# Performance work log

Measured on AMD Instinct MI355X. Metric: run time of the kernel, lower is better.

## Reference

```python
import jax, jax.numpy as jnp
import numpy as np
import math

B, S, D_MODEL, D_K = 4, 4096, 1024, 256

def setup_inputs() -> dict:
    key = jax.random.key(0)
    ks = jax.random.split(key, 9)
    def xavier(k, shape):
        fan_out, fan_in = shape
        limit = math.sqrt(6.0 / (fan_in + fan_out))
        return jax.random.uniform(k, shape, jnp.float32, -limit, limit)
    return {
        "_q": jax.random.normal(ks[0], (B, S, D_MODEL), jnp.float32),
        "_k": jax.random.normal(ks[1], (B, S, D_MODEL), jnp.float32),
        "_v": jax.random.normal(ks[2], (B, S, D_MODEL), jnp.float32),
        "mask": jnp.ones((B, 1, S), dtype=bool),  # unused by the original forward
        "Wq": xavier(ks[3], (D_K, D_MODEL)),
        "bq": jnp.zeros((D_K,), jnp.float32),
        "Wk": xavier(ks[4], (D_K, D_MODEL)),
        "bk": jnp.zeros((D_K,), jnp.float32),
        "Wv": xavier(ks[5], (D_K, D_MODEL)),
        "bv": jnp.zeros((D_K,), jnp.float32),
    }

def reference(_q, _k, _v, mask, Wq, bq, Wk, bk, Wv, bv):
    # Linear projections: x @ W.T + b  (torch nn.Linear semantics)
    q = jnp.einsum('bsm,km->bsk', _q, Wq) + bq  # [B,S,d_k]
    k = jnp.einsum('bsm,km->bsk', _k, Wk) + bk
    v = jnp.einsum('bsm,km->bsk', _v, Wv) + bv
    scores = jnp.einsum('bqk,bsk->bqs', q, k) / math.sqrt(D_K)  # [B,S,S]
    atten = jax.nn.softmax(scores, axis=-1)
    out = jnp.einsum('bqs,bsk->bqk', atten, v)  # [B,S,d_k]
    return out
```

## Files before the change

kernel.cpp:

```cpp
#include <hip/hip_runtime.h>
#include <stdint.h>

#define DEV static __device__ __forceinline__

typedef __bf16 bf16x8 __attribute__((ext_vector_type(8)));
typedef float f32x4 __attribute__((ext_vector_type(4)));

typedef const __attribute__((address_space(1))) void* as1cp;
typedef __attribute__((address_space(3))) void* as3p;

DEV uint32_t pk2(float lo, float hi) {
  uint16_t a = __builtin_bit_cast(uint16_t, (__bf16)lo);
  uint16_t b = __builtin_bit_cast(uint16_t, (__bf16)hi);
  return (uint32_t)a | ((uint32_t)b << 16);
}
DEV uint16_t bfc(float f) { return __builtin_bit_cast(uint16_t, (__bf16)f); }
DEV float bf2f(uint32_t h) { return __builtin_bit_cast(float, h << 16); }

DEV void gll16(const void* g, void* l) {
  __builtin_amdgcn_global_load_lds((as1cp)g, (as3p)l, 16, 0, 0);
}

__global__ __launch_bounds__(256, 3) void proj_kernel(
    const float* __restrict__ xq, const float* __restrict__ xk, const float* __restrict__ xv,
    const float* __restrict__ wq, const float* __restrict__ wk, const float* __restrict__ wv,
    const float* __restrict__ bq, const float* __restrict__ bk, const float* __restrict__ bv,
    uint16_t* __restrict__ qo, uint16_t* __restrict__ ko, uint16_t* __restrict__ vo)
{
  const int z = blockIdx.z;
  const float* X  = (z == 0) ? xq : (z == 1) ? xk : xv;
  const float* W  = (z == 0) ? wq : (z == 1) ? wk : wv;
  const float* Bi = (z == 0) ? bq : (z == 1) ? bk : bv;

  const int tid = threadIdx.x;
  const int lane = tid & 63;
  const int w = tid >> 6;
  const int wm = w >> 1, wn = w & 1;
  const int l15 = lane & 15, g = lane >> 4;
  const int m0 = blockIdx.x * 128;
  const int n0 = blockIdx.y * 128;

  __shared__ uint16_t sA[128 * 64];
  __shared__ uint16_t sB[128 * 64];

  const int srow = tid >> 4;
  const int scu  = tid & 15;
  const float* Abase = X + (size_t)(m0 + srow) * 1024 + scu * 4;
  const float* Wbase = W + (size_t)(n0 + srow) * 1024 + scu * 4;
  uint32_t sdst[8];
  #pragma unroll
  for (int r = 0; r < 8; ++r) {
    uint32_t row = (uint32_t)(r * 16 + srow);
    sdst[r] = row * 128 + (((uint32_t)scu * 8) ^ ((row & 7) << 4));
  }

  f32x4 acc[4][4];
  #pragma unroll
  for (int i = 0; i < 4; ++i)
    #pragma unroll
    for (int j = 0; j < 4; ++j) { f32x4 zz = {0.f, 0.f, 0.f, 0.f}; acc[i][j] = zz; }

  float4 a4[8];
  #pragma unroll
  for (int r = 0; r < 8; ++r)
    a4[r] = *(const float4*)(Abase + (size_t)r * 16384);

  for (int kt = 0; kt < 16; ++kt) {
    if (kt) __syncthreads();
    #pragma unroll
    for (int r = 0; r < 8; ++r) {
      uint2 p; p.x = pk2(a4[r].x, a4[r].y); p.y = pk2(a4[r].z, a4[r].w);
      *(uint2*)((char*)sA + sdst[r]) = p;
    }
    {
      float4 w4[8];
      #pragma unroll
      for (int r = 0; r < 8; ++r)
        w4[r] = *(const float4*)(Wbase + (size_t)r * 16384 + kt * 64);
      #pragma unroll
      for (int r = 0; r < 8; ++r) {
        uint2 p; p.x = pk2(w4[r].x, w4[r].y); p.y = pk2(w4[r].z, w4[r].w);
        *(uint2*)((char*)sB + sdst[r]) = p;
      }
    }
    __syncthreads();
    if (kt < 15) {
      #pragma unroll
      for (int r = 0; r < 8; ++r)
        a4[r] = *(const float4*)(Abase + (size_t)r * 16384 + (kt + 1) * 64);
    }
    #pragma unroll
    for (int ks = 0; ks < 2; ++ks) {
      bf16x8 fa[4], fb[4];
      #pragma unroll
      for (int f = 0; f < 4; ++f) {
        uint32_t row = wm * 64 + 16 * f + l15;
        fa[f] = *(const bf16x8*)((char*)sA + row * 128 +
                 (((uint32_t)(ks * 64 + g * 16)) ^ ((row & 7) << 4)));
      }
      #pragma unroll
      for (int f = 0; f < 4; ++f) {
        uint32_t row = wn * 64 + 16 * f + l15;
        fb[f] = *(const bf16x8*)((char*)sB + row * 128 +
                 (((uint32_t)(ks * 64 + g * 16)) ^ ((row & 7) << 4)));
      }
      #pragma unroll
      for (int fm = 0; fm < 4; ++fm)
        #pragma unroll
        for (int fn = 0; fn < 4; ++fn)
          acc[fm][fn] = __builtin_amdgcn_mfma_f32_16x16x32_bf16(fa[fm], fb[fn], acc[fm][fn], 0, 0, 0);
    }
  }

  #pragma unroll
  for (int fn = 0; fn < 4; ++fn) {
    const int n = n0 + wn * 64 + 16 * fn + l15;
    const float bias = Bi[n];
    #pragma unroll
    for (int fm = 0; fm < 4; ++fm) {
      const int mg = m0 + wm * 64 + 16 * fm + 4 * g;
      if (z == 0) {
        #pragma unroll
        for (int r = 0; r < 4; ++r)
          qo[(size_t)(mg + r) * 256 + n] =
              bfc((acc[fm][fn][r] + bias) * 0.09016844f);
      } else if (z == 1) {
        #pragma unroll
        for (int r = 0; r < 4; ++r)
          ko[(size_t)(mg + r) * 256 + n] = bfc(acc[fm][fn][r] + bias);
      } else {
        uint2 pv;
        pv.x = pk2(acc[fm][fn][0] + bias, acc[fm][fn][1] + bias);
        pv.y = pk2(acc[fm][fn][2] + bias, acc[fm][fn][3] + bias);
        *(uint2*)(vo + (((size_t)(mg >> 12)) << 20) + (((size_t)n) << 12) + (mg & 4095)) = pv;
      }
    }
  }
}

__global__ __launch_bounds__(512) void attn_kernel(
    const uint16_t* __restrict__ qg, const uint16_t* __restrict__ kg,
    const uint16_t* __restrict__ vg, float* __restrict__ out)
{
  extern __shared__ char smem[];

  const int bid = blockIdx.x;
  const int xcd = bid & 7, slot = bid >> 3;
  const int batch = xcd >> 1;
  const int q0 = (((xcd & 1) << 5) + slot) * 64;

  const int tid = threadIdx.x;
  const int lane = tid & 63;
  const int w = tid >> 6;
  const int hv = w >> 2;
  const int wq = w & 3;
  const int l15 = lane & 15, g = lane >> 4;
  const size_t rowb = (size_t)batch * 4096;

  bf16x8 qf[8];
  {
    const uint16_t* qp = qg + (rowb + q0 + wq * 16 + l15) * 256;
    #pragma unroll
    for (int ks = 0; ks < 8; ++ks) qf[ks] = *(const bf16x8*)(qp + ks * 32 + g * 8);
  }

  f32x4 o[16];
  #pragma unroll
  for (int i = 0; i < 16; ++i) { f32x4 zz = {0.f, 0.f, 0.f, 0.f}; o[i] = zz; }
  float mrow[4], lrow[4];
  #pragma unroll
  for (int r = 0; r < 4; ++r) { mrow[r] = -1e30f; lrow[r] = 0.f; }

  const char* kgb = (const char*)(kg + rowb * 256);
  const char* vgb = (const char*)(vg + (size_t)batch * 256 * 4096);

  uint32_t kOff[2][2], vOff[2][2], dOff[2];
  #pragma unroll
  for (int i = 0; i < 2; ++i) {
    uint32_t L = (uint32_t)(i * 512 + tid) * 16;
    dOff[i] = L;
    uint32_t row = L >> 9;
    uint32_t colsw = (L & 511) ^ ((row & 7) << 4);
    uint32_t fd = L >> 10, g2 = (L >> 8) & 3, lv = (L >> 4) & 15;
    #pragma unroll
    for (int h = 0; h < 2; ++h) {
      kOff[h][i] = (h * 32 + row) * 512 + colsw;
      vOff[h][i] = (fd * 16 + lv) * 8192 + (h * 32 + g2 * 8) * 2;
    }
  }

  auto STAGE = [&](int buf, int t) {
    const char* kt_ = kgb + (size_t)t * 32768;
    const char* vt_ = vgb + (size_t)t * 128;
    #pragma unroll
    for (int h = 0; h < 2; ++h) {
      char* kd = smem + (size_t)(h * 2 + buf) * 16384;
      char* vd = smem + 65536 + (size_t)(h * 2 + buf) * 16384;
      #pragma unroll
      for (int i = 0; i < 2; ++i) {
        gll16(kt_ + kOff[h][i], kd + dOff[i]);
        gll16(vt_ + vOff[h][i], vd + dOff[i]);
      }
    }
  };

  STAGE(0, 0);
  int buf = 0;
  const int hb = hv * 2;
  char* Pw = smem + 131072 + (size_t)w * 1024;

  for (int t = 0; t < 64; ++t) {
    __syncthreads();
    if (t + 1 < 64) STAGE(buf ^ 1, t + 1);

    const char* Kb = smem + (size_t)(hb + buf) * 16384;
    const char* Vb = smem + 65536 + (size_t)(hb + buf) * 16384;

    f32x4 s4[2];
    #pragma unroll
    for (int f = 0; f < 2; ++f) { f32x4 zz = {0.f, 0.f, 0.f, 0.f}; s4[f] = zz; }
    #pragma unroll
    for (int ks = 0; ks < 8; ++ks) {
      bf16x8 kf[2];
      #pragma unroll
      for (int f = 0; f < 2; ++f) {
        uint32_t row = 16 * f + l15;
        kf[f] = *(const bf16x8*)(Kb + row * 512 +
                 (((uint32_t)(ks * 64 + g * 16)) ^ ((l15 & 7) << 4)));
      }
      #pragma unroll
      for (int f = 0; f < 2; ++f)
        s4[f] = __builtin_amdgcn_mfma_f32_16x16x32_bf16(qf[ks], kf[f], s4[f], 0, 0, 0);
    }

    float mx[4];
    #pragma unroll
    for (int r = 0; r < 4; ++r) {
      float m2 = fmaxf(s4[0][r], s4[1][r]);
      m2 = fmaxf(m2, __shfl_xor(m2, 1, 64));
      m2 = fmaxf(m2, __shfl_xor(m2, 2, 64));
      m2 = fmaxf(m2, __shfl_xor(m2, 4, 64));
      m2 = fmaxf(m2, __shfl_xor(m2, 8, 64));
      mx[r] = m2;
    }
    int stable = (mx[0] <= mrow[0] + 8.f) && (mx[1] <= mrow[1] + 8.f) &&
                 (mx[2] <= mrow[2] + 8.f) && (mx[3] <= mrow[3] + 8.f);
    if (!__all(stable)) {
      float sc[4];
      #pragma unroll
      for (int r = 0; r < 4; ++r) {
        float mn = fmaxf(mrow[r], mx[r]);
        sc[r] = exp2f(mrow[r] - mn);
        mrow[r] = mn;
        lrow[r] *= sc[r];
      }
      #pragma unroll
      for (int j = 0; j < 16; ++j)
        #pragma unroll
        for (int r = 0; r < 4; ++r) o[j][r] *= sc[r];
    }
    float ps[2][4];
    #pragma unroll
    for (int r = 0; r < 4; ++r) {
      float sum = 0.f;
      #pragma unroll
      for (int f = 0; f < 2; ++f) { ps[f][r] = exp2f(s4[f][r] - mrow[r]); sum += ps[f][r]; }
      sum += __shfl_xor(sum, 1, 64);
      sum += __shfl_xor(sum, 2, 64);
      sum += __shfl_xor(sum, 4, 64);
      sum += __shfl_xor(sum, 8, 64);
      lrow[r] += sum;
    }

    #pragma unroll
    for (int f = 0; f < 2; ++f)
      #pragma unroll
      for (int r = 0; r < 4; ++r)
        *(uint16_t*)(Pw + (4 * g + r) * 64 +
            (((uint32_t)(32 * f + 2 * l15)) ^ ((uint32_t)g << 4))) = bfc(ps[f][r]);

    bf16x8 pa = *(const bf16x8*)(Pw + l15 * 64 + 16 * (g ^ (l15 >> 2)));
    #pragma unroll
    for (int fd = 0; fd < 16; ++fd) {
      bf16x8 vbf = *(const bf16x8*)(Vb + fd * 1024 + lane * 16);
      o[fd] = __builtin_amdgcn_mfma_f32_16x16x32_bf16(pa, vbf, o[fd], 0, 0, 0);
    }

    buf ^= 1;
  }

  float*    mlb = (float*)smem;
  uint32_t* ob  = (uint32_t*)(smem + 8192);
  __syncthreads();
  if (hv == 1) {
    #pragma unroll
    for (int r = 0; r < 4; ++r) {
      mlb[((0 * 4 + wq) * 64 + lane) * 4 + r] = mrow[r];
      mlb[((1 * 4 + wq) * 64 + lane) * 4 + r] = lrow[r];
    }
    #pragma unroll
    for (int fd = 0; fd < 16; ++fd)
      #pragma unroll
      for (int p = 0; p < 2; ++p)
        ob[(wq * 32 + fd * 2 + p) * 64 + lane] = pk2(o[fd][2 * p], o[fd][2 * p + 1]);
  }
  __syncthreads();
  if (hv == 0) {
    float a[4], b2[4], inv[4];
    #pragma unroll
    for (int r = 0; r < 4; ++r) {
      float mu = mlb[((0 * 4 + wq) * 64 + lane) * 4 + r];
      float lu = mlb[((1 * 4 + wq) * 64 + lane) * 4 + r];
      float mn = fmaxf(mrow[r], mu);
      a[r]  = exp2f(mrow[r] - mn);
      b2[r] = exp2f(mu - mn);
      inv[r] = 1.f / (lrow[r] * a[r] + lu * b2[r]);
    }
    float* op = out + (rowb + q0 + wq * 16) * 256;
    #pragma unroll
    for (int fd = 0; fd < 16; ++fd) {
      #pragma unroll
      for (int p = 0; p < 2; ++p) {
        uint32_t u = ob[(wq * 32 + fd * 2 + p) * 64 + lane];
        float vlo = bf2f(u & 0xffffu), vhi = bf2f(u >> 16);
        int r0 = 2 * p, r1 = 2 * p + 1;
        op[(4 * g + r0) * 256 + 16 * fd + l15] =
            (o[fd][r0] * a[r0] + vlo * b2[r0]) * inv[r0];
        op[(4 * g + r1) * 256 + 16 * fd + l15] =
            (o[fd][r1] * a[r1] + vhi * b2[r1]) * inv[r1];
      }
    }
  }
}

extern "C" void kernel_launch(void* const* d_in, const int* in_sizes, int n_in,
                              void* d_out, int out_size, void* d_ws, size_t ws_size,
                              hipStream_t stream) {
  const float* xq = (const float*)d_in[0];
  const float* xk = (const float*)d_in[1];
  const float* xv = (const float*)d_in[2];
  const float* wq = (const float*)d_in[4];
  const float* bq = (const float*)d_in[5];
  const float* wk = (const float*)d_in[6];
  const float* bk = (const float*)d_in[7];
  const float* wv = (const float*)d_in[8];
  const float* bv = (const float*)d_in[9];

  uint16_t* qws = (uint16_t*)d_ws;
  uint16_t* kws = qws + (size_t)4 * 4096 * 256;
  uint16_t* vws = kws + (size_t)4 * 4096 * 256;

  proj_kernel<<<dim3(128, 2, 3), 256, 0, stream>>>(
      xq, xk, xv, wq, wk, wv, bq, bk, bv, qws, kws, vws);

  (void)hipFuncSetAttribute((const void*)attn_kernel,
                            hipFuncAttributeMaxDynamicSharedMemorySize, 139264);
  attn_kernel<<<dim3(256), 512, 139264, stream>>>(qws, kws, vws, (float*)d_out);
}
```

Before: 435.0 us.

## Restructure attention to 32-query blocks with 32x32 MFMA and direct-global V loads

Attention now runs 512 blocks of 128 threads, each handling 32 queries with two waves that split the key range. S^T is computed with 32x32x16 MFMA and P is kept in registers through lane shuffles instead of passing through LDS. V fragments are read straight from global memory rather than staged, and K staging becomes single-buffered with two barriers per iteration. The two halves are merged through LDS with coalesced float4 output stores. LDS use drops sharply, allowing more blocks per CU, but this gives up K/V double-buffer overlap and may expose global V load latency.

```diff
diff --git a/kernel.cpp b/kernel.cpp
--- a/kernel.cpp
+++ b/kernel.cpp
@@ -5,6 +5,8 @@
 
 typedef __bf16 bf16x8 __attribute__((ext_vector_type(8)));
 typedef float f32x4 __attribute__((ext_vector_type(4)));
+typedef float f32x16 __attribute__((ext_vector_type(16)));
+typedef uint32_t u32x4 __attribute__((ext_vector_type(4)));
 
 typedef const __attribute__((address_space(1))) void* as1cp;
 typedef __attribute__((address_space(3))) void* as3p;
@@ -138,7 +140,7 @@
   }
 }
 
-__global__ __launch_bounds__(512) void attn_kernel(
+__global__ __launch_bounds__(128, 2) void attn_kernel(
     const uint16_t* __restrict__ qg, const uint16_t* __restrict__ kg,
     const uint16_t* __restrict__ vg, float* __restrict__ out)
 {
@@ -147,188 +149,149 @@
   const int bid = blockIdx.x;
   const int xcd = bid & 7, slot = bid >> 3;
   const int batch = xcd >> 1;
-  const int q0 = (((xcd & 1) << 5) + slot) * 64;
+  const int q0 = ((xcd & 1) * 64 + slot) * 32;
 
   const int tid = threadIdx.x;
   const int lane = tid & 63;
-  const int w = tid >> 6;
-  const int hv = w >> 2;
-  const int wq = w & 3;
-  const int l15 = lane & 15, g = lane >> 4;
+  const int hv = tid >> 6;
+  const int l31 = lane & 31, hh = lane >> 5;
   const size_t rowb = (size_t)batch * 4096;
 
-  bf16x8 qf[8];
+  bf16x8 qf[16];
   {
-    const uint16_t* qp = qg + (rowb + q0 + wq * 16 + l15) * 256;
-    #pragma unroll
-    for (int ks = 0; ks < 8; ++ks) qf[ks] = *(const bf16x8*)(qp + ks * 32 + g * 8);
-  }
-
-  f32x4 o[16];
-  #pragma unroll
-  for (int i = 0; i < 16; ++i) { f32x4 zz = {0.f, 0.f, 0.f, 0.f}; o[i] = zz; }
-  float mrow[4], lrow[4];
-  #pragma unroll
-  for (int r = 0; r < 4; ++r) { mrow[r] = -1e30f; lrow[r] = 0.f; }
-
-  const char* kgb = (const char*)(kg + rowb * 256);
-  const char* vgb = (const char*)(vg + (size_t)batch * 256 * 4096);
-
-  uint32_t kOff[2][2], vOff[2][2], dOff[2];
-  #pragma unroll
-  for (int i = 0; i < 2; ++i) {
-    uint32_t L = (uint32_t)(i * 512 + tid) * 16;
-    dOff[i] = L;
-    uint32_t row = L >> 9;
-    uint32_t colsw = (L & 511) ^ ((row & 7) << 4);
-    uint32_t fd = L >> 10, g2 = (L >> 8) & 3, lv = (L >> 4) & 15;
-    #pragma unroll
-    for (int h = 0; h < 2; ++h) {
-      kOff[h][i] = (h * 32 + row) * 512 + colsw;
-      vOff[h][i] = (fd * 16 + lv) * 8192 + (h * 32 + g2 * 8) * 2;
-    }
-  }
-
-  auto STAGE = [&](int buf, int t) {
-    const char* kt_ = kgb + (size_t)t * 32768;
-    const char* vt_ = vgb + (size_t)t * 128;
-    #pragma unroll
-    for (int h = 0; h < 2; ++h) {
-      char* kd = smem + (size_t)(h * 2 + buf) * 16384;
-      char* vd = smem + 65536 + (size_t)(h * 2 + buf) * 16384;
-      #pragma unroll
-      for (int i = 0; i < 2; ++i) {
-        gll16(kt_ + kOff[h][i], kd + dOff[i]);
-        gll16(vt_ + vOff[h][i], vd + dOff[i]);
-      }
+    const char* qp = (const char*)qg + (rowb + q0 + l31) * 512 + hh * 16;
+    #pragma unroll
+    for (int s = 0; s < 16; ++s) qf[s] = *(const bf16x8*)(qp + s * 32);
+  }
+
+  f32x16 o[8];
+  #pragma unroll
+  for (int i = 0; i < 8; ++i) { f32x16 zz = {}; o[i] = zz; }
+  float mrow = -1e30f, lrow = 0.f;
+
+  const char* kgb = (const char*)kg + rowb * 512;
+  const char* vgb = (const char*)vg + (size_t)batch * 2097152;
+
+  auto STAGE = [&](int t) {
+    #pragma unroll
+    for (int r = 0; r < 16; ++r) {
+      const int half = r >> 3;
+      uint32_t row = (uint32_t)(4 * r + (tid >> 5)) & 31u;
+      uint32_t colsw = (((uint32_t)(tid & 31)) * 16u) ^ (row << 4);
+      const char* src = kgb + (((size_t)(half * 2048 + t * 32) + row) << 9) + colsw;
+      gll16(src, smem + (size_t)(r * 128 + tid) * 16);
     }
   };
 
-  STAGE(0, 0);
-  int buf = 0;
-  const int hb = hv * 2;
-  char* Pw = smem + 131072 + (size_t)w * 1024;
+  STAGE(0);
+  __syncthreads();
+
+  const char* Kb = smem + hv * 16384;
+  const char* vLane = vgb + (size_t)l31 * 8192 + hv * 4096 + hh * 16;
+  const uint32_t csw = (uint32_t)l31 << 4;
 
   for (int t = 0; t < 64; ++t) {
+    f32x16 s4 = {};
+    const char* kr = Kb + (uint32_t)l31 * 512;
+    #pragma unroll
+    for (int s = 0; s < 16; ++s) {
+      bf16x8 kf = *(const bf16x8*)(kr + (((uint32_t)(32 * s + 16 * hh)) ^ csw));
+      s4 = __builtin_amdgcn_mfma_f32_32x32x16_bf16(kf, qf[s], s4, 0, 0, 0);
+    }
+
+    float pm = s4[0];
+    #pragma unroll
+    for (int r = 1; r < 16; ++r) pm = fmaxf(pm, s4[r]);
+    pm = fmaxf(pm, __shfl_xor(pm, 32, 64));
+    if (!__all(pm <= mrow + 8.f)) {
+      float mn = fmaxf(mrow, pm);
+      float sc = exp2f(mrow - mn);
+      lrow *= sc; mrow = mn;
+      #pragma unroll
+      for (int i = 0; i < 8; ++i) o[i] *= sc;
+    }
+    float p[16], sum = 0.f;
+    #pragma unroll
+    for (int r = 0; r < 16; ++r) { p[r] = exp2f(s4[r] - mrow); sum += p[r]; }
+    lrow += sum + __shfl_xor(sum, 32, 64);
+
+    uint32_t W[8], SW[8];
+    #pragma unroll
+    for (int i = 0; i < 8; ++i) W[i] = pk2(p[2 * i], p[2 * i + 1]);
+    #pragma unroll
+    for (int i = 0; i < 8; ++i) SW[i] = __shfl_xor(W[i], 32, 64);
+    u32x4 f0, f1;
+    if (hh == 0) {
+      f0 = (u32x4){W[0], W[1], SW[0], SW[1]};
+      f1 = (u32x4){W[4], W[5], SW[4], SW[5]};
+    } else {
+      f0 = (u32x4){SW[2], SW[3], W[2], W[3]};
+      f1 = (u32x4){SW[6], SW[7], W[6], W[7]};
+    }
+    bf16x8 pb0 = __builtin_bit_cast(bf16x8, f0);
+    bf16x8 pb1 = __builtin_bit_cast(bf16x8, f1);
+
+    const char* vt = vLane + t * 64;
+    #pragma unroll
+    for (int db = 0; db < 8; ++db) {
+      bf16x8 v0 = *(const bf16x8*)(vt + (size_t)db * 262144);
+      bf16x8 v1 = *(const bf16x8*)(vt + (size_t)db * 262144 + 32);
+      o[db] = __builtin_amdgcn_mfma_f32_32x32x16_bf16(v0, pb0, o[db], 0, 0, 0);
+      o[db] = __builtin_amdgcn_mfma_f32_32x32x16_bf16(v1, pb1, o[db], 0, 0, 0);
+    }
+
     __syncthreads();
-    if (t + 1 < 64) STAGE(buf ^ 1, t + 1);
-
-    const char* Kb = smem + (size_t)(hb + buf) * 16384;
-    const char* Vb = smem + 65536 + (size_t)(hb + buf) * 16384;
-
-    f32x4 s4[2];
-    #pragma unroll
-    for (int f = 0; f < 2; ++f) { f32x4 zz = {0.f, 0.f, 0.f, 0.f}; s4[f] = zz; }
-    #pragma unroll
-    for (int ks = 0; ks < 8; ++ks) {
-      bf16x8 kf[2];
-      #pragma unroll
-      for (int f = 0; f < 2; ++f) {
-        uint32_t row = 16 * f + l15;
-        kf[f] = *(const bf16x8*)(Kb + row * 512 +
-                 (((uint32_t)(ks * 64 + g * 16)) ^ ((l15 & 7) << 4)));
-      }
-      #pragma unroll
-      for (int f = 0; f < 2; ++f)
-        s4[f] = __builtin_amdgcn_mfma_f32_16x16x32_bf16(qf[ks], kf[f], s4[f], 0, 0, 0);
-    }
-
-    float mx[4];
-    #pragma unroll
-    for (int r = 0; r < 4; ++r) {
-      float m2 = fmaxf(s4[0][r], s4[1][r]);
-      m2 = fmaxf(m2, __shfl_xor(m2, 1, 64));
-      m2 = fmaxf(m2, __shfl_xor(m2, 2, 64));
-      m2 = fmaxf(m2, __shfl_xor(m2, 4, 64));
-      m2 = fmaxf(m2, __shfl_xor(m2, 8, 64));
-      mx[r] = m2;
-    }
-    int stable = (mx[0] <= mrow[0] + 8.f) && (mx[1] <= mrow[1] + 8.f) &&
-                 (mx[2] <= mrow[2] + 8.f) && (mx[3] <= mrow[3] + 8.f);
-    if (!__all(stable)) {
-      float sc[4];
-      #pragma unroll
-      for (int r = 0; r < 4; ++r) {
-        float mn = fmaxf(mrow[r], mx[r]);
-        sc[r] = exp2f(mrow[r] - mn);
-        mrow[r] = mn;
-        lrow[r] *= sc[r];
-      }
-      #pragma unroll
-      for (int j = 0; j < 16; ++j)
-        #pragma unroll
-        for (int r = 0; r < 4; ++r) o[j][r] *= sc[r];
-    }
-    float ps[2][4];
-    #pragma unroll
-    for (int r = 0; r < 4; ++r) {
-      float sum = 0.f;
-      #pragma unroll
-      for (int f = 0; f < 2; ++f) { ps[f][r] = exp2f(s4[f][r] - mrow[r]); sum += ps[f][r]; }
-      sum += __shfl_xor(sum, 1, 64);
-      sum += __shfl_xor(sum, 2, 64);
-      sum += __shfl_xor(sum, 4, 64);
-      sum += __shfl_xor(sum, 8, 64);
-      lrow[r] += sum;
-    }
-
-    #pragma unroll
-    for (int f = 0; f < 2; ++f)
-      #pragma unroll
-      for (int r = 0; r < 4; ++r)
-        *(uint16_t*)(Pw + (4 * g + r) * 64 +
-            (((uint32_t)(32 * f + 2 * l15)) ^ ((uint32_t)g << 4))) = bfc(ps[f][r]);
-
-    bf16x8 pa = *(const bf16x8*)(Pw + l15 * 64 + 16 * (g ^ (l15 >> 2)));
-    #pragma unroll
-    for (int fd = 0; fd < 16; ++fd) {
-      bf16x8 vbf = *(const bf16x8*)(Vb + fd * 1024 + lane * 16);
-      o[fd] = __builtin_amdgcn_mfma_f32_16x16x32_bf16(pa, vbf, o[fd], 0, 0, 0);
-    }
-
-    buf ^= 1;
-  }
-
-  float*    mlb = (float*)smem;
-  uint32_t* ob  = (uint32_t*)(smem + 8192);
+    if (t < 63) STAGE(t + 1);
+    __syncthreads();
+  }
+
+  {
+    char* Ob = smem + hv * 16384;
+    #pragma unroll
+    for (int db = 0; db < 8; ++db)
+      #pragma unroll
+      for (int k = 0; k < 4; ++k) {
+        uint32_t d2 = (uint32_t)(db * 64 + k * 16 + hh * 8);
+        uint2 wv2;
+        wv2.x = pk2(o[db][4 * k + 0], o[db][4 * k + 1]);
+        wv2.y = pk2(o[db][4 * k + 2], o[db][4 * k + 3]);
+        *(uint2*)(Ob + (uint32_t)l31 * 512 + (d2 ^ csw)) = wv2;
+      }
+    float* mls = (float*)(smem + 32768);
+    if (hh == 0) {
+      mls[(hv * 32 + l31) * 2 + 0] = mrow;
+      mls[(hv * 32 + l31) * 2 + 1] = lrow;
+    }
+  }
   __syncthreads();
-  if (hv == 1) {
-    #pragma unroll
-    for (int r = 0; r < 4; ++r) {
-      mlb[((0 * 4 + wq) * 64 + lane) * 4 + r] = mrow[r];
-      mlb[((1 * 4 + wq) * 64 + lane) * 4 + r] = lrow[r];
-    }
-    #pragma unroll
-    for (int fd = 0; fd < 16; ++fd)
-      #pragma unroll
-      for (int p = 0; p < 2; ++p)
-        ob[(wq * 32 + fd * 2 + p) * 64 + lane] = pk2(o[fd][2 * p], o[fd][2 * p + 1]);
-  }
-  __syncthreads();
-  if (hv == 0) {
-    float a[4], b2[4], inv[4];
-    #pragma unroll
-    for (int r = 0; r < 4; ++r) {
-      float mu = mlb[((0 * 4 + wq) * 64 + lane) * 4 + r];
-      float lu = mlb[((1 * 4 + wq) * 64 + lane) * 4 + r];
-      float mn = fmaxf(mrow[r], mu);
-      a[r]  = exp2f(mrow[r] - mn);
-      b2[r] = exp2f(mu - mn);
-      inv[r] = 1.f / (lrow[r] * a[r] + lu * b2[r]);
-    }
-    float* op = out + (rowb + q0 + wq * 16) * 256;
-    #pragma unroll
-    for (int fd = 0; fd < 16; ++fd) {
-      #pragma unroll
-      for (int p = 0; p < 2; ++p) {
-        uint32_t u = ob[(wq * 32 + fd * 2 + p) * 64 + lane];
-        float vlo = bf2f(u & 0xffffu), vhi = bf2f(u >> 16);
-        int r0 = 2 * p, r1 = 2 * p + 1;
-        op[(4 * g + r0) * 256 + 16 * fd + l15] =
-            (o[fd][r0] * a[r0] + vlo * b2[r0]) * inv[r0];
-        op[(4 * g + r1) * 256 + 16 * fd + l15] =
-            (o[fd][r1] * a[r1] + vhi * b2[r1]) * inv[r1];
-      }
+
+  {
+    const float* mls = (const float*)(smem + 32768);
+    const int q = tid >> 2, c = tid & 3;
+    float m0 = mls[q * 2], l0 = mls[q * 2 + 1];
+    float m1 = mls[64 + q * 2], l1 = mls[64 + q * 2 + 1];
+    float mn = fmaxf(m0, m1);
+    float a0 = exp2f(m0 - mn), a1 = exp2f(m1 - mn);
+    float inv = 1.f / (l0 * a0 + l1 * a1);
+    a0 *= inv; a1 *= inv;
+    float* op = out + (rowb + q0 + q) * 256;
+    const uint32_t qs = (uint32_t)q << 4;
+    #pragma unroll
+    for (int j = 0; j < 8; ++j) {
+      uint32_t d2 = (uint32_t)(c * 128 + 16 * j);
+      uint4 u0 = *(const uint4*)(smem + (uint32_t)q * 512 + (d2 ^ qs));
+      uint4 u1 = *(const uint4*)(smem + 16384 + (uint32_t)q * 512 + (d2 ^ qs));
+      float4 r0, r1;
+      r0.x = bf2f(u0.x & 0xffffu) * a0 + bf2f(u1.x & 0xffffu) * a1;
+      r0.y = bf2f(u0.x >> 16)     * a0 + bf2f(u1.x >> 16)     * a1;
+      r0.z = bf2f(u0.y & 0xffffu) * a0 + bf2f(u1.y & 0xffffu) * a1;
+      r0.w = bf2f(u0.y >> 16)     * a0 + bf2f(u1.y >> 16)     * a1;
+      r1.x = bf2f(u0.z & 0xffffu) * a0 + bf2f(u1.z & 0xffffu) * a1;
+      r1.y = bf2f(u0.z >> 16)     * a0 + bf2f(u1.z >> 16)     * a1;
+      r1.z = bf2f(u0.w & 0xffffu) * a0 + bf2f(u1.w & 0xffffu) * a1;
+      r1.w = bf2f(u0.w >> 16)     * a0 + bf2f(u1.w >> 16)     * a1;
+      *(float4*)(op + c * 64 + 8 * j) = r0;
+      *(float4*)(op + c * 64 + 8 * j + 4) = r1;
     }
   }
 }
@@ -354,6 +317,6 @@
       xq, xk, xv, wq, wk, wv, bq, bk, bv, qws, kws, vws);
 
   (void)hipFuncSetAttribute((const void*)attn_kernel,
-                            hipFuncAttributeMaxDynamicSharedMemorySize, 139264);
-  attn_kernel<<<dim3(256), 512, 139264, stream>>>(qws, kws, vws, (float*)d_out);
-}
+                            hipFuncAttributeMaxDynamicSharedMemorySize, 33280);
+  attn_kernel<<<dim3(512), 128, 33280, stream>>>(qws, kws, vws, (float*)d_out);
+}
```

After: 555.2 us. 27.6% more time.
